# Kernel tuning notes

Measured on AMD Instinct MI355X. Metric: run time of the kernel, lower is better.

The kernel has to match this reference:

```python
import jax, jax.numpy as jnp
import numpy as np

B, To, Tw, D = 96, 50, 40, 512


def setup_inputs() -> dict:
    key = jax.random.key(0)
    ko, kw = jax.random.split(key)
    o = jax.random.normal(ko, (B, To, D), dtype=jnp.float32)
    w = jax.random.normal(kw, (B, Tw, D), dtype=jnp.float32)
    return {"o": o, "w": w}


def reference(o, w):
    # o: (Bo, To, D) box features; w: (Bw, Tw, D) caption word features.
    # fo/fw are KVIdentity => Ko=Vo=o, Kw=Vw=w.
    d = o.shape[-1]
    scale = 1.0 / jnp.sqrt(jnp.asarray(d, dtype=o.dtype))
    # cross-batch attention scores: (Bw, Bo, Tw, To)
    att = jnp.einsum('wtd,bod->wbto', w, o) * scale
    att = jax.nn.softmax(att, axis=3)           # softmax over To (boxes)
    # attended object values: (Bw, Bo, Tw, D)
    att_vo = jnp.einsum('wbto,bod->wbtd', att, o)
    # word-object compatibility logits: (Bw, Bo, Tw)
    logits = jnp.einsum('wbtd,wtd->wbt', att_vo, w)
    logp = jax.nn.log_softmax(logits, axis=1)    # contrast over Bo
    per_pair = jnp.mean(logp, axis=2)            # (Bw, Bo)
    loss = -jnp.mean(jnp.diagonal(per_pair))
    return loss
```

## Files before the change

### kernel.cpp

```cpp
#include <hip/hip_runtime.h>
#include <cstdint>
#include <cstddef>

typedef unsigned short u16;
typedef __attribute__((ext_vector_type(8))) short short8;
typedef __attribute__((ext_vector_type(8))) unsigned short u16x8;
typedef __attribute__((ext_vector_type(4))) float f32x4;

#define NB   96
#define TO   50
#define TW   40
#define DD   512
#define MROWS (NB*TW)
#define BM   128
#define BK   32
#define NKC  (DD/BK)

#define WBF_OFF   0u
#define OBF_OFF   (MROWS*DD*2u)
#define LOG_OFF   (OBF_OFF + NB*TO*DD*2u)
#define ZB_OFF    (LOG_OFF + NB*NB*TW*4u)
#define PART_OFF  (ZB_OFF + 256u)

__device__ __forceinline__ u16 f2bf(float f) {
  unsigned int u = __builtin_bit_cast(unsigned int, f);
  u += 0x7fffu + ((u >> 16) & 1u);
  return (u16)(u >> 16);
}

__device__ __forceinline__ void gload16(const void* g, void* l) {
  __builtin_amdgcn_global_load_lds(
      (__attribute__((address_space(1))) unsigned int*)(g),
      (__attribute__((address_space(3))) unsigned int*)(l), 16, 0, 0);
}

__global__ void k_convert(const float* __restrict__ o, const float* __restrict__ w,
                          u16* __restrict__ obf, u16* __restrict__ wbf,
                          u16* __restrict__ zbuf) {
  const int stride = gridDim.x * blockDim.x;
  const int tid0 = blockIdx.x * blockDim.x + threadIdx.x;
  const int no8 = NB*TO*DD/8;
  const int nw8 = NB*TW*DD/8;
  for (int i = tid0; i < no8; i += stride) {
    const float4* s = (const float4*)o + (size_t)i*2;
    float4 a = s[0], b = s[1];
    u16x8 r = { f2bf(a.x), f2bf(a.y), f2bf(a.z), f2bf(a.w),
                f2bf(b.x), f2bf(b.y), f2bf(b.z), f2bf(b.w) };
    *(u16x8*)(obf + (size_t)i*8) = r;
  }
  for (int i = tid0; i < nw8; i += stride) {
    const float4* s = (const float4*)w + (size_t)i*2;
    float4 a = s[0], b = s[1];
    u16x8 r = { f2bf(a.x), f2bf(a.y), f2bf(a.z), f2bf(a.w),
                f2bf(b.x), f2bf(b.y), f2bf(b.z), f2bf(b.w) };
    *(u16x8*)(wbf + (size_t)i*8) = r;
  }
  if (tid0 < 16) {
    u16x8 z = {0,0,0,0,0,0,0,0};
    *(u16x8*)(zbuf + tid0*8) = z;
  }
}

__global__ void __launch_bounds__(256) k_main(
    const u16* __restrict__ wbf, const u16* __restrict__ obf,
    const u16* __restrict__ zbuf, float* __restrict__ logits) {
  __shared__ u16 ldsA[2][BM*BK];
  __shared__ u16 ldsB[2][BM*BK];
  const int tid  = threadIdx.x;
  const int lane = tid & 63;
  const int wid  = tid >> 6;
  const int r0   = blockIdx.y * BM;
  const int ob0  = blockIdx.x * 2;

  const u16* gA[2];
  const u16* gB[2];
  bool realB[2];
  #pragma unroll
  for (int i = 0; i < 2; ++i) {
    int c   = i*256 + tid;
    int row = c >> 2;
    int kc8 = (c & 3) * 8;
    gA[i] = wbf + (size_t)(r0 + row) * DD + kc8;
    int ob = ob0 + (row >> 6);
    int oo = row & 63;
    realB[i] = (oo < TO);
    gB[i] = realB[i] ? (obf + ((size_t)ob * TO + oo) * DD + kc8) : zbuf;
  }
  const int ldst = (wid * 64) * 8;

  auto stage = [&](int buf, int k0) {
    #pragma unroll
    for (int i = 0; i < 2; ++i) {
      gload16(gA[i] + k0, &ldsA[buf][i*2048 + ldst]);
      gload16(realB[i] ? gB[i] + k0 : gB[i], &ldsB[buf][i*2048 + ldst]);
    }
  };

  const int wr   = (wid >> 1) * 64;
  const int wc   = (wid & 1) * 64;
  const int lrow = lane & 15;
  const int lk   = (lane >> 4) * 8;

  f32x4 zero4 = {0.f, 0.f, 0.f, 0.f};
  f32x4 acc[4][4];
  #pragma unroll
  for (int mi = 0; mi < 4; ++mi)
    #pragma unroll
    for (int ni = 0; ni < 4; ++ni) acc[mi][ni] = zero4;

  stage(0, 0);
  for (int kc = 0; kc < NKC; ++kc) {
    const int cur = kc & 1;
    __syncthreads();
    if (kc + 1 < NKC) stage(cur ^ 1, (kc + 1) * BK);
    short8 af[4], bfr[4];
    #pragma unroll
    for (int mi = 0; mi < 4; ++mi)
      af[mi] = *(const short8*)&ldsA[cur][(wr + mi*16 + lrow) * BK + lk];
    #pragma unroll
    for (int ni = 0; ni < 4; ++ni)
      bfr[ni] = *(const short8*)&ldsB[cur][(wc + ni*16 + lrow) * BK + lk];
    #pragma unroll
    for (int mi = 0; mi < 4; ++mi)
      #pragma unroll
      for (int ni = 0; ni < 4; ++ni)
        acc[mi][ni] = __builtin_amdgcn_mfma_f32_16x16x32_bf16(
            af[mi], bfr[ni], acc[mi][ni], 0, 0, 0);
  }

  const float scale = 0.04419417382415922f;
  const int ob = ob0 + (wid & 1);
  #pragma unroll
  for (int mi = 0; mi < 4; ++mi) {
    #pragma unroll
    for (int q = 0; q < 4; ++q) {
      float v0 = acc[mi][0][q], v1 = acc[mi][1][q],
            v2 = acc[mi][2][q], v3 = acc[mi][3][q];
      float m = fmaxf(fmaxf(v0, v1), v2);
      if (lrow < 2) m = fmaxf(m, v3);
      #pragma unroll
      for (int d = 1; d < 16; d <<= 1) m = fmaxf(m, __shfl_xor(m, d));
      float p0 = __expf((v0 - m) * scale);
      float p1 = __expf((v1 - m) * scale);
      float p2 = __expf((v2 - m) * scale);
      float den = p0 + p1 + p2;
      float num = p0*v0 + p1*v1 + p2*v2;
      if (lrow < 2) {
        float p3 = __expf((v3 - m) * scale);
        den += p3; num += p3*v3;
      }
      #pragma unroll
      for (int d = 1; d < 16; d <<= 1) {
        den += __shfl_xor(den, d);
        num += __shfl_xor(num, d);
      }
      if (lrow == 0) {
        int row = r0 + wr + mi*16 + (lane >> 4)*4 + q;
        int wb = row / TW, t = row - wb*TW;
        logits[((size_t)wb*NB + ob)*TW + t] = num / den;
      }
    }
  }
}

__global__ void k_lse(const float* __restrict__ logits, double* __restrict__ partial) {
  const int wb = blockIdx.x;
  const int t  = threadIdx.x;
  double val = 0.0;
  if (t < TW) {
    const float* base = logits + (size_t)wb*NB*TW + t;
    float m = -1e30f;
    for (int ob = 0; ob < NB; ++ob) m = fmaxf(m, base[(size_t)ob*TW]);
    float den = 0.f;
    for (int ob = 0; ob < NB; ++ob) den += __expf(base[(size_t)ob*TW] - m);
    val = (double)(base[(size_t)wb*TW] - m - __logf(den));
  }
  for (int d = 32; d > 0; d >>= 1) val += __shfl_down(val, d);
  if (t == 0) partial[wb] = val;
}

__global__ void k_out(const double* __restrict__ partial, float* __restrict__ out) {
  const int t = threadIdx.x;
  double v = partial[t];
  if (t < 32) v += partial[t + 64];
  for (int d = 32; d > 0; d >>= 1) v += __shfl_down(v, d);
  if (t == 0) out[0] = (float)(-v / (double)(NB*TW));
}

extern "C" void kernel_launch(void* const* d_in, const int* in_sizes, int n_in,
                              void* d_out, int out_size, void* d_ws, size_t ws_size,
                              hipStream_t stream) {
  const float* o = (const float*)d_in[0];
  const float* w = (const float*)d_in[1];
  char* ws = (char*)d_ws;
  u16*    wbf     = (u16*)(ws + WBF_OFF);
  u16*    obf     = (u16*)(ws + OBF_OFF);
  float*  logits  = (float*)(ws + LOG_OFF);
  u16*    zbuf    = (u16*)(ws + ZB_OFF);
  double* partial = (double*)(ws + PART_OFF);

  k_convert<<<1200, 256, 0, stream>>>(o, w, obf, wbf, zbuf);
  dim3 g1(NB/2, MROWS/BM);
  k_main<<<g1, 256, 0, stream>>>(wbf, obf, zbuf, logits);
  k_lse<<<NB, 64, 0, stream>>>(logits, partial);
  k_out<<<1, 64, 0, stream>>>(partial, (float*)d_out);
}
```

Measured before the change: 127.4 us.

## Transpose logits layout, parallelize log-softmax per row, and fuse final reduction via atomics

```diff
diff --git a/kernel.cpp b/kernel.cpp
--- a/kernel.cpp
+++ b/kernel.cpp
@@ -19,8 +19,7 @@
 #define WBF_OFF   0u
 #define OBF_OFF   (MROWS*DD*2u)
 #define LOG_OFF   (OBF_OFF + NB*TO*DD*2u)
-#define ZB_OFF    (LOG_OFF + NB*NB*TW*4u)
-#define PART_OFF  (ZB_OFF + 256u)
+#define ZB_OFF    (LOG_OFF + MROWS*NB*4u)
 
 __device__ __forceinline__ u16 f2bf(float f) {
   unsigned int u = __builtin_bit_cast(unsigned int, f);
@@ -36,7 +35,7 @@
 
 __global__ void k_convert(const float* __restrict__ o, const float* __restrict__ w,
                           u16* __restrict__ obf, u16* __restrict__ wbf,
-                          u16* __restrict__ zbuf) {
+                          u16* __restrict__ zbuf, float* __restrict__ out) {
   const int stride = gridDim.x * blockDim.x;
   const int tid0 = blockIdx.x * blockDim.x + threadIdx.x;
   const int no8 = NB*TO*DD/8;
@@ -59,6 +58,7 @@
     u16x8 z = {0,0,0,0,0,0,0,0};
     *(u16x8*)(zbuf + tid0*8) = z;
   }
+  if (tid0 == 0) out[0] = 0.f;
 }
 
 __global__ void __launch_bounds__(256) k_main(
@@ -156,35 +156,32 @@
       }
       if (lrow == 0) {
         int row = r0 + wr + mi*16 + (lane >> 4)*4 + q;
-        int wb = row / TW, t = row - wb*TW;
-        logits[((size_t)wb*NB + ob)*TW + t] = num / den;
+        logits[(size_t)row * NB + ob] = num / den;
       }
     }
   }
 }
 
-__global__ void k_lse(const float* __restrict__ logits, double* __restrict__ partial) {
-  const int wb = blockIdx.x;
-  const int t  = threadIdx.x;
-  double val = 0.0;
-  if (t < TW) {
-    const float* base = logits + (size_t)wb*NB*TW + t;
-    float m = -1e30f;
-    for (int ob = 0; ob < NB; ++ob) m = fmaxf(m, base[(size_t)ob*TW]);
-    float den = 0.f;
-    for (int ob = 0; ob < NB; ++ob) den += __expf(base[(size_t)ob*TW] - m);
-    val = (double)(base[(size_t)wb*TW] - m - __logf(den));
-  }
-  for (int d = 32; d > 0; d >>= 1) val += __shfl_down(val, d);
-  if (t == 0) partial[wb] = val;
-}
-
-__global__ void k_out(const double* __restrict__ partial, float* __restrict__ out) {
-  const int t = threadIdx.x;
-  double v = partial[t];
-  if (t < 32) v += partial[t + 64];
-  for (int d = 32; d > 0; d >>= 1) v += __shfl_down(v, d);
-  if (t == 0) out[0] = (float)(-v / (double)(NB*TW));
+__global__ void __launch_bounds__(256) k_lse(
+    const float* __restrict__ logits, float* __restrict__ out) {
+  const int tid  = threadIdx.x;
+  const int lane = tid & 63;
+  const int wid  = tid >> 6;
+  const int row  = blockIdx.x * 4 + wid;
+  const float* base = logits + (size_t)row * NB;
+  float v0 = base[lane];
+  float v1 = (lane < NB - 64) ? base[64 + lane] : -1e30f;
+  float m = fmaxf(v0, v1);
+  #pragma unroll
+  for (int d = 1; d < 64; d <<= 1) m = fmaxf(m, __shfl_xor(m, d));
+  float den = __expf(v0 - m) + ((lane < NB - 64) ? __expf(v1 - m) : 0.f);
+  #pragma unroll
+  for (int d = 1; d < 64; d <<= 1) den += __shfl_xor(den, d);
+  if (lane == 0) {
+    const int wb = row / TW;
+    float logp = base[wb] - m - __logf(den);
+    atomicAdd(out, logp * (-1.0f / (float)MROWS));
+  }
 }
 
 extern "C" void kernel_launch(void* const* d_in, const int* in_sizes, int n_in,
@@ -197,11 +194,9 @@
   u16*    obf     = (u16*)(ws + OBF_OFF);
   float*  logits  = (float*)(ws + LOG_OFF);
   u16*    zbuf    = (u16*)(ws + ZB_OFF);
-  double* partial = (double*)(ws + PART_OFF);
-
-  k_convert<<<1200, 256, 0, stream>>>(o, w, obf, wbf, zbuf);
+
+  k_convert<<<1200, 256, 0, stream>>>(o, w, obf, wbf, zbuf, (float*)d_out);
   dim3 g1(NB/2, MROWS/BM);
   k_main<<<g1, 256, 0, stream>>>(wbf, obf, zbuf, logits);
-  k_lse<<<NB, 64, 0, stream>>>(logits, partial);
-  k_out<<<1, 64, 0, stream>>>(partial, (float*)d_out);
-}
+  k_lse<<<960, 256, 0, stream>>>(logits, (float*)d_out);
+}
```

Measured after the change: 158.3 us. 1.24x slower.
